# Optimization experiments

Measured on AMD Instinct MI355X. Metric: run time of the kernel, lower is better.

The kernel has to match this reference:

```python
import jax, jax.numpy as jnp
import numpy as np
from jax import lax

B, T = 1024, 1000
EPS = 1e-3  # keras BatchNormalization default epsilon
ALPHA = 0.2  # tf.nn.leaky_relu default alpha


def setup_inputs() -> dict:
    key = jax.random.key(0)
    ks = jax.random.split(key, 40)
    f32 = jnp.float32
    n = lambda k, s, sc=0.1: jax.random.normal(k, s, dtype=f32) * sc
    inp = {"x": jax.random.normal(ks[0], (B, 2, T, 1), dtype=f32)}
    # main conv stack (HWIO kernels)
    inp["c1k"] = n(ks[1], (1, 5, 1, 10));  inp["c1b"] = n(ks[2], (10,), 0.01)
    inp["c2k"] = n(ks[3], (1, 5, 10, 10)); inp["c2b"] = n(ks[4], (10,), 0.01)
    inp["c3k"] = n(ks[5], (1, 5, 10, 10)); inp["c3b"] = n(ks[6], (10,), 0.01)
    inp["c4k"] = n(ks[7], (2, 1, 10, 20)); inp["c4b"] = n(ks[8], (20,), 0.01)
    # batchnorm (inference) params
    for i, k0 in zip((1, 2, 3), (9, 13, 17)):
        inp[f"g{i}"]  = 1.0 + n(ks[k0], (10,), 0.05)
        inp[f"be{i}"] = n(ks[k0 + 1], (10,), 0.05)
        inp[f"m{i}"]  = n(ks[k0 + 2], (10,), 0.05)
        inp[f"v{i}"]  = 1.0 + jax.random.uniform(ks[k0 + 3], (10,), dtype=f32) * 0.1
    # dense head: flatten of [B,1,T-12,20]
    inp["dns_w"] = n(ks[21], ((T - 12) * 20, 1), 0.02)
    inp["dns_b"] = jnp.zeros((1,), f32)
    # MHRSSA blocks: 10 heads of Conv2D(2,(2,1)) stacked -> K [10,2,Cin,2], b [10,2];
    # depthwise (1,5) over 10 channels -> dw [5,10], db [10]
    inp["a1K"] = n(ks[22], (10, 2, 1, 2));  inp["a1b"] = n(ks[23], (10, 2), 0.01)
    inp["a1dw"] = n(ks[24], (5, 10));       inp["a1db"] = n(ks[25], (10,), 0.01)
    inp["a2K"] = n(ks[26], (10, 2, 10, 2)); inp["a2b"] = n(ks[27], (10, 2), 0.01)
    inp["a2dw"] = n(ks[28], (5, 10));       inp["a2db"] = n(ks[29], (10,), 0.01)
    inp["a3K"] = n(ks[30], (10, 2, 10, 2)); inp["a3b"] = n(ks[31], (10, 2), 0.01)
    inp["a3dw"] = n(ks[32], (5, 10));       inp["a3db"] = n(ks[33], (10,), 0.01)
    return inp


def conv2d(x, k, b):
    return lax.conv_general_dilated(x, k, (1, 1), 'VALID',
                                    dimension_numbers=('NHWC', 'HWIO', 'NHWC')) + b


def bn_inf(x, g, be, m, v):
    return (x - m) * (g * lax.rsqrt(v + EPS)) + be


def lrelu(x):
    return jnp.where(x >= 0, x, ALPHA * x)


def mhrssa(x, K, b, dw, db):
    # x: [B,2,T,C]; K: [10,2,C,2] (10 heads of a (2,1)-valid conv) -> [B,10,T,2]
    m = jnp.einsum('bhtc,ihco->bito', x, K) + b[None, :, None, :]
    a = jnp.transpose(m, (0, 3, 2, 1))  # [B,2,T,10]
    Tt = a.shape[2]
    # depthwise (1,5) valid conv over time, per-channel taps dw[w,i]
    y = sum(a[:, :, w:w + Tt - 4, :] * dw[w] for w in range(5)) + db
    return jax.nn.softmax(y, axis=-1)


def reference(x, c1k, c1b, g1, be1, m1, v1, c2k, c2b, g2, be2, m2, v2,
              c3k, c3b, g3, be3, m3, v3, c4k, c4b, dns_w, dns_b,
              a1K, a1b, a1dw, a1db, a2K, a2b, a2dw, a2db, a3K, a3b, a3dw, a3db):
    att1 = mhrssa(x, a1K, a1b, a1dw, a1db)
    h = lrelu(bn_inf(conv2d(x, c1k, c1b), g1, be1, m1, v1)) * att1
    att2 = mhrssa(h, a2K, a2b, a2dw, a2db)
    h = lrelu(bn_inf(conv2d(h, c2k, c2b), g2, be2, m2, v2)) * att2
    att3 = mhrssa(h, a3K, a3b, a3dw, a3db)
    h = lrelu(bn_inf(conv2d(h, c3k, c3b), g3, be3, m3, v3)) * att3
    h = lrelu(conv2d(h, c4k, c4b))          # [B,1,T-12,20]
    h = h.reshape(h.shape[0], -1)
    return h @ dns_w + dns_b                # RGS mode: raw scalar output
```

## Files before the change

kernel.cpp:

```cpp
#include <hip/hip_runtime.h>

#define REP10(X) X(0) X(1) X(2) X(3) X(4) X(5) X(6) X(7) X(8) X(9)
#define REP5(X)  X(0) X(1) X(2) X(3) X(4)

typedef __attribute__((ext_vector_type(2))) float v2;

__device__ __forceinline__ void fold_stage(
    float* dst, const float* g, const float* be, const float* mn,
    const float* vr, const float* cb, const float* adw, const float* adb,
    const float* aK, const float* ab, int CIN)
{
  const int tid = threadIdx.x;
  if (tid < 10) {
    const float sc = g[tid] * rsqrtf(vr[tid] + 1e-3f);
    dst[tid]      = sc;
    dst[10 + tid] = (cb[tid] - mn[tid]) * sc + be[tid];
    dst[70 + tid] = adb[tid] * 1.44269504088896340736f;
  }
  if (tid >= 10 && tid < 60)
    dst[10 + tid] = adw[tid - 10] * 1.44269504088896340736f;
  if (tid < 20)
    dst[80 + tid] = ab[(tid % 10) * 2 + tid / 10];
  const int n = 2 * CIN * 2 * 10;
  for (int idx = tid; idx < n; idx += 64) {
    const int i  = idx % 10;
    const int r  = idx / 10;
    const int o  = r % 2;
    const int r2 = r / 2;
    const int ci = r2 % CIN;
    const int h  = r2 / CIN;
    dst[100 + idx] = aK[((i * 2 + h) * CIN + ci) * 2 + o];
  }
}

__global__ void prep_kernel(
    const float* g1, const float* be1, const float* m1, const float* v1,
    const float* cb1, const float* a1dw, const float* a1db,
    const float* a1K, const float* a1b,
    const float* g2, const float* be2, const float* m2, const float* v2_,
    const float* cb2, const float* a2dw, const float* a2db,
    const float* a2K, const float* a2b,
    const float* g3, const float* be3, const float* m3, const float* v3,
    const float* cb3, const float* a3dw, const float* a3db,
    const float* a3K, const float* a3b,
    float* consts)
{
  fold_stage(consts,        g1, be1, m1, v1,  cb1, a1dw, a1db, a1K, a1b, 1);
  fold_stage(consts + 512,  g2, be2, m2, v2_, cb2, a2dw, a2db, a2K, a2b, 10);
  fold_stage(consts + 1024, g3, be3, m3, v3,  cb3, a3dw, a3db, a3K, a3b, 10);
}

__global__ void transpose_dnsw(const float* __restrict__ dnsw,
                               float* __restrict__ dnswT)
{
  const int cc = blockIdx.x;
  for (int t = threadIdx.x; t < 988; t += 256)
    dnswT[cc * 988 + t] = dnsw[t * 20 + cc];
}

template <int CIN>
__global__ __launch_bounds__(128) void stage_kernel(
    const float* __restrict__ in, float* __restrict__ outp, int Tout,
    const float* __restrict__ ck, const float* __restrict__ cst)
{
  __shared__ float smm[10][136];
  const int tid = threadIdx.x;
  const int o   = blockIdx.y;
  const int t0  = blockIdx.x * 128;
  const int Tin = Tout + 4;
  const float* __restrict__ inb = in + (size_t)blockIdx.z * (CIN * 2000);

  const float* __restrict__ scale  = cst;
  const float* __restrict__ shift2 = cst + 10;
  const float* __restrict__ adw2   = cst + 20;
  const float* __restrict__ adb2   = cst + 70;
  const float* __restrict__ abp    = cst + 80;
  const float* __restrict__ aKp    = cst + 100;

  for (int lt = tid; lt < 132; lt += 128) {
    const int t = t0 + lt;
    if (t < Tin) {
#define DECLM(p) v2 mp##p = *reinterpret_cast<const v2*>(abp + o * 10 + 2 * p);
      REP5(DECLM)
#undef DECLM
#pragma unroll
      for (int h = 0; h < 2; ++h)
#pragma unroll
        for (int ci = 0; ci < CIN; ++ci) {
          const float xin = inb[(ci * 2 + h) * 1000 + t];
          const float* kb = aKp + ((h * CIN + ci) * 2 + o) * 10;
#define FMAM(p) mp##p += xin * *reinterpret_cast<const v2*>(kb + 2 * p);
          REP5(FMAM)
#undef FMAM
        }
#define STM(p) smm[2 * p][lt] = mp##p.x; smm[2 * p + 1][lt] = mp##p.y;
      REP5(STM)
#undef STM
    }
  }
  __syncthreads();

  const int tt = t0 + tid;
  if (tt >= Tout) return;

#define DECLY(p) v2 yp##p = *reinterpret_cast<const v2*>(adb2 + 2 * p);
  REP5(DECLY)
#undef DECLY
#pragma unroll
  for (int w = 0; w < 5; ++w) {
    const float* aw = adw2 + w * 10;
#define FMAY(p) { const v2 sv = {smm[2 * p][tid + w], smm[2 * p + 1][tid + w]}; \
    yp##p += sv * *reinterpret_cast<const v2*>(aw + 2 * p); }
    REP5(FMAY)
#undef FMAY
  }

#define DECLA(p) v2 ap##p = {0.f, 0.f};
  REP5(DECLA)
#undef DECLA
  const float* __restrict__ cinb = inb + o * 1000 + tt;
#pragma unroll
  for (int w = 0; w < 5; ++w)
#pragma unroll
    for (int ci = 0; ci < CIN; ++ci) {
      const float xin = cinb[ci * 2000 + w];
      const float* kb = ck + (w * CIN + ci) * 10;
#define FMAC(p) ap##p += xin * *reinterpret_cast<const v2*>(kb + 2 * p);
      REP5(FMAC)
#undef FMAC
    }

  const float y0 = yp0.x, y1 = yp0.y, y2 = yp1.x, y3 = yp1.y, y4 = yp2.x,
              y5 = yp2.y, y6 = yp3.x, y7 = yp3.y, y8 = yp4.x, y9 = yp4.y;
  float mx = y0;
  mx = fmaxf(mx, y1); mx = fmaxf(mx, y2); mx = fmaxf(mx, y3);
  mx = fmaxf(mx, y4); mx = fmaxf(mx, y5); mx = fmaxf(mx, y6);
  mx = fmaxf(mx, y7); mx = fmaxf(mx, y8); mx = fmaxf(mx, y9);
#define DECLE(i) const float e##i = exp2f(y##i - mx);
  REP10(DECLE)
#undef DECLE
  const float sm  = e0 + e1 + e2 + e3 + e4 + e5 + e6 + e7 + e8 + e9;
  const float inv = __builtin_amdgcn_rcpf(sm);

  const float a0 = ap0.x, a1 = ap0.y, a2 = ap1.x, a3 = ap1.y, a4 = ap2.x,
              a5 = ap2.y, a6 = ap3.x, a7 = ap3.y, a8 = ap4.x, a9 = ap4.y;
  float* __restrict__ ob = outp + (size_t)blockIdx.z * 20000 + o * 1000 + tt;
#define STO(i) { float bv = a##i * scale[i] + shift2[i];                       \
    bv = fmaxf(bv, 0.2f * bv);                                                 \
    ob[i * 2000] = bv * e##i * inv; }
  REP10(STO)
#undef STO
}

__global__ __launch_bounds__(256) void final_kernel(
    const float* __restrict__ h3, const float* __restrict__ c4k,
    const float* __restrict__ c4b, const float* __restrict__ dnswT,
    const float* __restrict__ dnsb, float* __restrict__ outp, int b0)
{
  __shared__ float red[4];
  const int tid = threadIdx.x;
  const float* __restrict__ hb = h3 + (size_t)blockIdx.x * 20000;
  float partial = 0.f;
#pragma unroll 1
  for (int t = 2 * tid; t < 988; t += 512) {
#define LOADH(i)                                                               \
    const float2 xa##i = *reinterpret_cast<const float2*>(hb + i*2000 + t);    \
    const float2 xb##i = *reinterpret_cast<const float2*>(hb + i*2000 + 1000 + t);
    REP10(LOADH)
#undef LOADH
    float d0 = 0.f, d1 = 0.f;
#pragma unroll 4
    for (int cc = 0; cc < 20; ++cc) {
      const float bias = c4b[cc];
      float a0 = bias, a1 = bias;
#define FMA4(i) { const float wA = c4k[i*20 + cc], wB = c4k[(10+i)*20 + cc];   \
      a0 += xa##i.x * wA + xb##i.x * wB; a1 += xa##i.y * wA + xb##i.y * wB; }
      REP10(FMA4)
#undef FMA4
      a0 = fmaxf(a0, 0.2f * a0); a1 = fmaxf(a1, 0.2f * a1);
      const float2 dT = *reinterpret_cast<const float2*>(dnswT + cc * 988 + t);
      d0 += a0 * dT.x; d1 += a1 * dT.y;
    }
    partial += d0 + d1;
  }
#pragma unroll
  for (int off = 32; off > 0; off >>= 1)
    partial += __shfl_down(partial, off, 64);
  if ((tid & 63) == 0) red[tid >> 6] = partial;
  __syncthreads();
  if (tid == 0)
    outp[b0 + blockIdx.x] = red[0] + red[1] + red[2] + red[3] + dnsb[0];
}

extern "C" void kernel_launch(void* const* d_in, const int* in_sizes, int n_in,
                              void* d_out, int out_size, void* d_ws, size_t ws_size,
                              hipStream_t stream) {
  const float* p[35];
  for (int i = 0; i < 35; ++i) p[i] = (const float*)d_in[i];
  const int B = in_sizes[0] / 2000;

  float* consts = (float*)d_ws;
  float* dnswT  = consts + 1536;
  float* hA     = consts + 21296;
  const size_t avail = ws_size - 21296u * 4u;
  int CH = 1024;
  if (CH > B) CH = B;
  while ((size_t)CH * 160000ull > avail && CH > 1) CH >>= 1;
  float* hB = hA + (size_t)CH * 20000;

  prep_kernel<<<dim3(1), dim3(64), 0, stream>>>(
      p[9], p[10], p[11], p[12], p[2], p[25], p[26], p[23], p[24],
      p[13], p[14], p[15], p[16], p[4], p[29], p[30], p[27], p[28],
      p[17], p[18], p[19], p[20], p[6], p[33], p[34], p[31], p[32],
      consts);
  transpose_dnsw<<<dim3(20), dim3(256), 0, stream>>>(p[21], dnswT);

  for (int b0 = 0; b0 < B; b0 += CH) {
    const int cc = (B - b0 < CH) ? (B - b0) : CH;
    stage_kernel<1><<<dim3(8, 2, cc), dim3(128), 0, stream>>>(
        p[0] + (size_t)b0 * 2000, hA, 996, p[1], consts);
    stage_kernel<10><<<dim3(8, 2, cc), dim3(128), 0, stream>>>(
        hA, hB, 992, p[3], consts + 512);
    stage_kernel<10><<<dim3(8, 2, cc), dim3(128), 0, stream>>>(
        hB, hA, 988, p[5], consts + 1024);
    final_kernel<<<dim3(cc), dim3(256), 0, stream>>>(
        hA, p[7], p[8], dnswT, p[22], (float*)d_out, b0);
  }
}
```

Before: 179.7 us.

## Fuse all conv/attention stages and dense head into one halo-tiled kernel

New measurement: 717.3 us. +299.3%, slower.

```diff
diff --git a/kernel.cpp b/kernel.cpp
--- a/kernel.cpp
+++ b/kernel.cpp
@@ -4,6 +4,12 @@
 #define REP5(X)  X(0) X(1) X(2) X(3) X(4)
 
 typedef __attribute__((ext_vector_type(2))) float v2;
+
+#define SXB 140
+#define SH1 140
+#define SH2 136
+#define SH3 128
+#define SMM 140
 
 __device__ __forceinline__ void fold_stage(
     float* dst, const float* g, const float* be, const float* mn,
@@ -50,138 +56,157 @@
   fold_stage(consts + 1024, g3, be3, m3, v3,  cb3, a3dw, a3db, a3K, a3b, 10);
 }
 
-__global__ void transpose_dnsw(const float* __restrict__ dnsw,
-                               float* __restrict__ dnswT)
-{
-  const int cc = blockIdx.x;
-  for (int t = threadIdx.x; t < 988; t += 256)
-    dnswT[cc * 988 + t] = dnsw[t * 20 + cc];
-}
-
 template <int CIN>
-__global__ __launch_bounds__(128) void stage_kernel(
-    const float* __restrict__ in, float* __restrict__ outp, int Tout,
+__device__ __forceinline__ void ein_phase(
+    const float* __restrict__ src, int sstride,
+    float* __restrict__ smm, int Lm, const float* __restrict__ cst)
+{
+  const float* __restrict__ abp = cst + 80;
+  const float* __restrict__ aKp = cst + 100;
+  for (int idx = threadIdx.x; idx < 2 * Lm; idx += 256) {
+    const int o  = (idx >= Lm) ? 1 : 0;
+    const int lt = idx - o * Lm;
+#define DECLM(p) v2 mp##p = *reinterpret_cast<const v2*>(abp + o * 10 + 2 * p);
+    REP5(DECLM)
+#undef DECLM
+#pragma unroll
+    for (int h = 0; h < 2; ++h)
+#pragma unroll
+      for (int ci = 0; ci < CIN; ++ci) {
+        const float xin = src[(ci * 2 + h) * sstride + lt];
+        const float* kb = aKp + ((h * CIN + ci) * 2 + o) * 10;
+#define FMAM(p) mp##p += xin * *reinterpret_cast<const v2*>(kb + 2 * p);
+        REP5(FMAM)
+#undef FMAM
+      }
+#define STM(p) smm[(4 * p + o) * SMM + lt]     = mp##p.x;                      \
+               smm[(4 * p + 2 + o) * SMM + lt] = mp##p.y;
+    REP5(STM)
+#undef STM
+  }
+}
+
+template <int CIN>
+__device__ __forceinline__ void h_phase(
+    const float* __restrict__ src, int sstride,
+    const float* __restrict__ smm,
+    float* __restrict__ dst, int dstride, int Lh,
     const float* __restrict__ ck, const float* __restrict__ cst)
 {
-  __shared__ float smm[10][136];
-  const int tid = threadIdx.x;
-  const int o   = blockIdx.y;
-  const int t0  = blockIdx.x * 128;
-  const int Tin = Tout + 4;
-  const float* __restrict__ inb = in + (size_t)blockIdx.z * (CIN * 2000);
-
   const float* __restrict__ scale  = cst;
   const float* __restrict__ shift2 = cst + 10;
   const float* __restrict__ adw2   = cst + 20;
   const float* __restrict__ adb2   = cst + 70;
-  const float* __restrict__ abp    = cst + 80;
-  const float* __restrict__ aKp    = cst + 100;
-
-  for (int lt = tid; lt < 132; lt += 128) {
-    const int t = t0 + lt;
-    if (t < Tin) {
-#define DECLM(p) v2 mp##p = *reinterpret_cast<const v2*>(abp + o * 10 + 2 * p);
-      REP5(DECLM)
-#undef DECLM
-#pragma unroll
-      for (int h = 0; h < 2; ++h)
-#pragma unroll
-        for (int ci = 0; ci < CIN; ++ci) {
-          const float xin = inb[(ci * 2 + h) * 1000 + t];
-          const float* kb = aKp + ((h * CIN + ci) * 2 + o) * 10;
-#define FMAM(p) mp##p += xin * *reinterpret_cast<const v2*>(kb + 2 * p);
-          REP5(FMAM)
-#undef FMAM
-        }
-#define STM(p) smm[2 * p][lt] = mp##p.x; smm[2 * p + 1][lt] = mp##p.y;
-      REP5(STM)
-#undef STM
+  for (int idx = threadIdx.x; idx < 2 * Lh; idx += 256) {
+    const int o  = (idx >= Lh) ? 1 : 0;
+    const int lt = idx - o * Lh;
+
+#define DECLY(p) v2 yp##p = *reinterpret_cast<const v2*>(adb2 + 2 * p);
+    REP5(DECLY)
+#undef DECLY
+#pragma unroll
+    for (int w = 0; w < 5; ++w) {
+      const float* aw = adw2 + w * 10;
+#define FMAY(p) { const v2 sv = {smm[(4 * p + o) * SMM + lt + w],              \
+                                 smm[(4 * p + 2 + o) * SMM + lt + w]};         \
+      yp##p += sv * *reinterpret_cast<const v2*>(aw + 2 * p); }
+      REP5(FMAY)
+#undef FMAY
     }
+
+#define DECLA(p) v2 ap##p = {0.f, 0.f};
+    REP5(DECLA)
+#undef DECLA
+#pragma unroll
+    for (int w = 0; w < 5; ++w)
+#pragma unroll
+      for (int ci = 0; ci < CIN; ++ci) {
+        const float xin = src[(ci * 2 + o) * sstride + lt + w];
+        const float* kb = ck + (w * CIN + ci) * 10;
+#define FMAC(p) ap##p += xin * *reinterpret_cast<const v2*>(kb + 2 * p);
+        REP5(FMAC)
+#undef FMAC
+      }
+
+    const float y0 = yp0.x, y1 = yp0.y, y2 = yp1.x, y3 = yp1.y, y4 = yp2.x,
+                y5 = yp2.y, y6 = yp3.x, y7 = yp3.y, y8 = yp4.x, y9 = yp4.y;
+    float mx = y0;
+    mx = fmaxf(mx, y1); mx = fmaxf(mx, y2); mx = fmaxf(mx, y3);
+    mx = fmaxf(mx, y4); mx = fmaxf(mx, y5); mx = fmaxf(mx, y6);
+    mx = fmaxf(mx, y7); mx = fmaxf(mx, y8); mx = fmaxf(mx, y9);
+#define DECLE(i) const float e##i = exp2f(y##i - mx);
+    REP10(DECLE)
+#undef DECLE
+    const float sm  = e0 + e1 + e2 + e3 + e4 + e5 + e6 + e7 + e8 + e9;
+    const float inv = __builtin_amdgcn_rcpf(sm);
+
+    const float a0 = ap0.x, a1 = ap0.y, a2 = ap1.x, a3 = ap1.y, a4 = ap2.x,
+                a5 = ap2.y, a6 = ap3.x, a7 = ap3.y, a8 = ap4.x, a9 = ap4.y;
+#define STO(i) { float bv = a##i * scale[i] + shift2[i];                       \
+      bv = fmaxf(bv, 0.2f * bv);                                               \
+      dst[(i * 2 + o) * dstride + lt] = bv * e##i * inv; }
+    REP10(STO)
+#undef STO
+  }
+}
+
+__global__ __launch_bounds__(256) void fused_kernel(
+    const float* __restrict__ x,
+    const float* __restrict__ c1k, const float* __restrict__ c2k,
+    const float* __restrict__ c3k, const float* __restrict__ c4k,
+    const float* __restrict__ c4b, const float* __restrict__ dnsw,
+    const float* __restrict__ cst, float* __restrict__ ws)
+{
+  __shared__ float xb[2 * SXB];
+  __shared__ float h1b[2800];
+  __shared__ float h2b[2720];
+  __shared__ float smm[2800];
+  __shared__ float red[4];
+
+  const int chunk = blockIdx.x;
+  const int b     = blockIdx.y;
+  const int T0    = chunk * 128;
+  const int L3    = min(128, 988 - T0);
+  const int L2 = L3 + 4, L1 = L3 + 8, LX = L3 + 12;
+  const int tid = threadIdx.x;
+
+  for (int idx = tid; idx < 2 * LX; idx += 256) {
+    const int h  = (idx >= LX) ? 1 : 0;
+    const int lt = idx - h * LX;
+    xb[h * SXB + lt] = x[(size_t)b * 2000 + h * 1000 + T0 + lt];
   }
   __syncthreads();
 
-  const int tt = t0 + tid;
-  if (tt >= Tout) return;
-
-#define DECLY(p) v2 yp##p = *reinterpret_cast<const v2*>(adb2 + 2 * p);
-  REP5(DECLY)
-#undef DECLY
-#pragma unroll
-  for (int w = 0; w < 5; ++w) {
-    const float* aw = adw2 + w * 10;
-#define FMAY(p) { const v2 sv = {smm[2 * p][tid + w], smm[2 * p + 1][tid + w]}; \
-    yp##p += sv * *reinterpret_cast<const v2*>(aw + 2 * p); }
-    REP5(FMAY)
-#undef FMAY
-  }
-
-#define DECLA(p) v2 ap##p = {0.f, 0.f};
-  REP5(DECLA)
-#undef DECLA
-  const float* __restrict__ cinb = inb + o * 1000 + tt;
-#pragma unroll
-  for (int w = 0; w < 5; ++w)
-#pragma unroll
-    for (int ci = 0; ci < CIN; ++ci) {
-      const float xin = cinb[ci * 2000 + w];
-      const float* kb = ck + (w * CIN + ci) * 10;
-#define FMAC(p) ap##p += xin * *reinterpret_cast<const v2*>(kb + 2 * p);
-      REP5(FMAC)
-#undef FMAC
-    }
-
-  const float y0 = yp0.x, y1 = yp0.y, y2 = yp1.x, y3 = yp1.y, y4 = yp2.x,
-              y5 = yp2.y, y6 = yp3.x, y7 = yp3.y, y8 = yp4.x, y9 = yp4.y;
-  float mx = y0;
-  mx = fmaxf(mx, y1); mx = fmaxf(mx, y2); mx = fmaxf(mx, y3);
-  mx = fmaxf(mx, y4); mx = fmaxf(mx, y5); mx = fmaxf(mx, y6);
-  mx = fmaxf(mx, y7); mx = fmaxf(mx, y8); mx = fmaxf(mx, y9);
-#define DECLE(i) const float e##i = exp2f(y##i - mx);
-  REP10(DECLE)
-#undef DECLE
-  const float sm  = e0 + e1 + e2 + e3 + e4 + e5 + e6 + e7 + e8 + e9;
-  const float inv = __builtin_amdgcn_rcpf(sm);
-
-  const float a0 = ap0.x, a1 = ap0.y, a2 = ap1.x, a3 = ap1.y, a4 = ap2.x,
-              a5 = ap2.y, a6 = ap3.x, a7 = ap3.y, a8 = ap4.x, a9 = ap4.y;
-  float* __restrict__ ob = outp + (size_t)blockIdx.z * 20000 + o * 1000 + tt;
-#define STO(i) { float bv = a##i * scale[i] + shift2[i];                       \
-    bv = fmaxf(bv, 0.2f * bv);                                                 \
-    ob[i * 2000] = bv * e##i * inv; }
-  REP10(STO)
-#undef STO
-}
-
-__global__ __launch_bounds__(256) void final_kernel(
-    const float* __restrict__ h3, const float* __restrict__ c4k,
-    const float* __restrict__ c4b, const float* __restrict__ dnswT,
-    const float* __restrict__ dnsb, float* __restrict__ outp, int b0)
-{
-  __shared__ float red[4];
-  const int tid = threadIdx.x;
-  const float* __restrict__ hb = h3 + (size_t)blockIdx.x * 20000;
+  ein_phase<1>(xb, SXB, smm, LX, cst);            __syncthreads();
+  h_phase<1>(xb, SXB, smm, h1b, SH1, L1, c1k, cst); __syncthreads();
+  ein_phase<10>(h1b, SH1, smm, L1, cst + 512);    __syncthreads();
+  h_phase<10>(h1b, SH1, smm, h2b, SH2, L2, c2k, cst + 512); __syncthreads();
+  ein_phase<10>(h2b, SH2, smm, L2, cst + 1024);   __syncthreads();
+  h_phase<10>(h2b, SH2, smm, h1b , SH3, L3, c3k, cst + 1024);
+  __syncthreads();
+
   float partial = 0.f;
-#pragma unroll 1
-  for (int t = 2 * tid; t < 988; t += 512) {
-#define LOADH(i)                                                               \
-    const float2 xa##i = *reinterpret_cast<const float2*>(hb + i*2000 + t);    \
-    const float2 xb##i = *reinterpret_cast<const float2*>(hb + i*2000 + 1000 + t);
-    REP10(LOADH)
-#undef LOADH
-    float d0 = 0.f, d1 = 0.f;
-#pragma unroll 4
-    for (int cc = 0; cc < 20; ++cc) {
-      const float bias = c4b[cc];
-      float a0 = bias, a1 = bias;
-#define FMA4(i) { const float wA = c4k[i*20 + cc], wB = c4k[(10+i)*20 + cc];   \
-      a0 += xa##i.x * wA + xb##i.x * wB; a1 += xa##i.y * wA + xb##i.y * wB; }
+  for (int idx = tid; idx < 2 * L3; idx += 256) {
+    const int hf = (idx >= L3) ? 1 : 0;
+    const int t  = idx - hf * L3;
+#define LDH(i) const float xa##i = h1b[(i * 2 + 0) * SH3 + t];                 \
+               const float xc##i = h1b[(i * 2 + 1) * SH3 + t];
+    REP10(LDH)
+#undef LDH
+    const float* __restrict__ dwp = dnsw + (size_t)(T0 + t) * 20 + hf * 10;
+    float dot = 0.f;
+#pragma unroll
+    for (int cc = 0; cc < 10; ++cc) {
+      const int ccg = hf * 10 + cc;
+      float acc = c4b[ccg];
+#define FMA4(i) acc += xa##i * c4k[i * 20 + ccg] +                             \
+                       xc##i * c4k[(10 + i) * 20 + ccg];
       REP10(FMA4)
 #undef FMA4
-      a0 = fmaxf(a0, 0.2f * a0); a1 = fmaxf(a1, 0.2f * a1);
-      const float2 dT = *reinterpret_cast<const float2*>(dnswT + cc * 988 + t);
-      d0 += a0 * dT.x; d1 += a1 * dT.y;
+      acc = fmaxf(acc, 0.2f * acc);
+      dot += acc * dwp[cc];
     }
-    partial += d0 + d1;
+    partial += dot;
   }
 #pragma unroll
   for (int off = 32; off > 0; off >>= 1)
@@ -189,7 +214,20 @@
   if ((tid & 63) == 0) red[tid >> 6] = partial;
   __syncthreads();
   if (tid == 0)
-    outp[b0 + blockIdx.x] = red[0] + red[1] + red[2] + red[3] + dnsb[0];
+    ws[(size_t)b * 8 + chunk] = red[0] + red[1] + red[2] + red[3];
+}
+
+__global__ void vignet_reduce(const float* __restrict__ ws,
+                              const float* __restrict__ dnsb,
+                              float* __restrict__ out, int B)
+{
+  const int b = blockIdx.x * blockDim.x + threadIdx.x;
+  if (b < B) {
+    float s = dnsb[0];
+#pragma unroll
+    for (int c = 0; c < 8; ++c) s += ws[b * 8 + c];
+    out[b] = s;
+  }
 }
 
 extern "C" void kernel_launch(void* const* d_in, const int* in_sizes, int n_in,
@@ -200,30 +238,17 @@
   const int B = in_sizes[0] / 2000;
 
   float* consts = (float*)d_ws;
-  float* dnswT  = consts + 1536;
-  float* hA     = consts + 21296;
-  const size_t avail = ws_size - 21296u * 4u;
-  int CH = 1024;
-  if (CH > B) CH = B;
-  while ((size_t)CH * 160000ull > avail && CH > 1) CH >>= 1;
-  float* hB = hA + (size_t)CH * 20000;
+  float* wspart = consts + 1536;
 
   prep_kernel<<<dim3(1), dim3(64), 0, stream>>>(
       p[9], p[10], p[11], p[12], p[2], p[25], p[26], p[23], p[24],
       p[13], p[14], p[15], p[16], p[4], p[29], p[30], p[27], p[28],
       p[17], p[18], p[19], p[20], p[6], p[33], p[34], p[31], p[32],
       consts);
-  transpose_dnsw<<<dim3(20), dim3(256), 0, stream>>>(p[21], dnswT);
-
-  for (int b0 = 0; b0 < B; b0 += CH) {
-    const int cc = (B - b0 < CH) ? (B - b0) : CH;
-    stage_kernel<1><<<dim3(8, 2, cc), dim3(128), 0, stream>>>(
-        p[0] + (size_t)b0 * 2000, hA, 996, p[1], consts);
-    stage_kernel<10><<<dim3(8, 2, cc), dim3(128), 0, stream>>>(
-        hA, hB, 992, p[3], consts + 512);
-    stage_kernel<10><<<dim3(8, 2, cc), dim3(128), 0, stream>>>(
-        hB, hA, 988, p[5], consts + 1024);
-    final_kernel<<<dim3(cc), dim3(256), 0, stream>>>(
-        hA, p[7], p[8], dnswT, p[22], (float*)d_out, b0);
-  }
-}
+
+  fused_kernel<<<dim3(8, B), dim3(256), 0, stream>>>(
+      p[0], p[1], p[3], p[5], p[7], p[8], p[21], consts, wspart);
+
+  vignet_reduce<<<dim3((B + 255) / 256), dim3(256), 0, stream>>>(
+      wspart, p[22], (float*)d_out, B);
+}
```
